# Performance work log

Hardware: AMD Instinct MI355X
Metric: run time of the kernel (lower is better)

## Reference

```python
import jax, jax.numpy as jnp
import numpy as np

NUM_HEADS = 16
NUM_KV_HEADS = 4
HEAD_DIM = 128
DIM = 2048
B, S = 2, 2048


def apply_rotary(t, cos, sin):
    # t: [B, S, H, D]; cos/sin: [S, D//2] -> broadcast [1, S, 1, D//2]
    tr = t.reshape(*t.shape[:-1], HEAD_DIM // 2, 2)
    t_r, t_i = tr[..., 0], tr[..., 1]
    c = cos[None, :, None, :]
    s = sin[None, :, None, :]
    o_r = t_r * c - t_i * s
    o_i = t_r * s + t_i * c
    return jnp.stack([o_r, o_i], axis=-1).reshape(t.shape)


def setup_inputs() -> dict:
    key = jax.random.key(0)
    ks = jax.random.split(key, 7)
    sc = 1.0 / np.sqrt(DIM)
    x = jax.random.normal(ks[0], (B, S, DIM), jnp.float32)
    pos = jnp.arange(S, dtype=jnp.float32)[:, None]
    inv_freq = 1.0 / (10000.0 ** (jnp.arange(0, HEAD_DIM, 2, dtype=jnp.float32) / HEAD_DIM))
    ang = pos * inv_freq[None, :]
    freqs_cos = jnp.cos(ang)
    freqs_sin = jnp.sin(ang)
    w_q = jax.random.normal(ks[1], (DIM, NUM_HEADS * HEAD_DIM), jnp.float32) * sc
    w_k = jax.random.normal(ks[2], (DIM, NUM_KV_HEADS * HEAD_DIM), jnp.float32) * sc
    w_v = jax.random.normal(ks[3], (DIM, NUM_KV_HEADS * HEAD_DIM), jnp.float32) * sc
    w_o = jax.random.normal(ks[4], (NUM_HEADS * HEAD_DIM, DIM), jnp.float32) * sc
    return {"x": x, "freqs_cos": freqs_cos, "freqs_sin": freqs_sin,
            "w_q": w_q, "w_k": w_k, "w_v": w_v, "w_o": w_o}


def reference(x, freqs_cos, freqs_sin, w_q, w_k, w_v, w_o):
    b, s, _ = x.shape
    kv_rep = NUM_HEADS // NUM_KV_HEADS
    q = (x @ w_q).reshape(b, s, NUM_HEADS, HEAD_DIM)
    k = (x @ w_k).reshape(b, s, NUM_KV_HEADS, HEAD_DIM)
    v = (x @ w_v).reshape(b, s, NUM_KV_HEADS, HEAD_DIM)
    q = apply_rotary(q, freqs_cos, freqs_sin)
    k = apply_rotary(k, freqs_cos, freqs_sin)
    # GQA: repeat KV heads to match query heads
    k = jnp.repeat(k, kv_rep, axis=2)
    v = jnp.repeat(v, kv_rep, axis=2)
    scores = jnp.einsum('bqhd,bkhd->bhqk', q, k) / np.sqrt(HEAD_DIM)
    causal = jnp.triu(jnp.full((s, s), -jnp.inf, jnp.float32), k=1)
    scores = scores + causal[None, None, :, :]
    attn = jax.nn.softmax(scores, axis=-1)
    out = jnp.einsum('bhqk,bkhd->bqhd', attn, v).reshape(b, s, NUM_HEADS * HEAD_DIM)
    return out @ w_o
```

## Files before the change

kernel.cpp:

```cpp
#include <hip/hip_runtime.h>
#include <stdint.h>

#define DIMSZ 2048
#define NH 16
#define NKV 4
#define HD 128
#define BATCH 2
#define SEQ 2048
#define MROWS (BATCH*SEQ)
#define NQKV (NH*HD + 2*NKV*HD)

typedef unsigned short u16;
typedef float f32x4 __attribute__((ext_vector_type(4)));
typedef short short8 __attribute__((ext_vector_type(8)));
typedef __bf16 bf16x8 __attribute__((ext_vector_type(8)));
typedef unsigned short u16x4 __attribute__((ext_vector_type(4)));

__device__ __forceinline__ u16 f2bf(float f) {
  __bf16 h = (__bf16)f;
  return __builtin_bit_cast(u16, h);
}

__device__ __forceinline__ float bf2f(u16 h) {
  union { uint32_t u; float f; } v; v.u = ((uint32_t)h) << 16; return v.f;
}

__device__ __forceinline__ void async16(void* lds, const void* g) {
  __builtin_amdgcn_global_load_lds(
      (const __attribute__((address_space(1))) void*)(g),
      (__attribute__((address_space(3))) void*)(lds), 16, 0, 0);
}

__device__ __forceinline__ bf16x8 load_frag(const u16* p) {
  short8 v = *reinterpret_cast<const short8*>(p);
  return __builtin_bit_cast(bf16x8, v);
}

__global__ void cast_x_kernel(const float* __restrict__ x, u16* __restrict__ xb) {
  int i = (blockIdx.x * blockDim.x + threadIdx.x) * 4;
  float4 v = *reinterpret_cast<const float4*>(x + i);
  u16x4 o;
  o.x = f2bf(v.x); o.y = f2bf(v.y); o.z = f2bf(v.z); o.w = f2bf(v.w);
  *reinterpret_cast<u16x4*>(xb + i) = o;
}

__global__ __launch_bounds__(1024) void wtrans_all_kernel(const float* __restrict__ wq,
                                                          const float* __restrict__ wk,
                                                          const float* __restrict__ wv,
                                                          const float* __restrict__ wo,
                                                          u16* __restrict__ wtqkv,
                                                          u16* __restrict__ wto) {
  __shared__ float t[32][33];
  int y = blockIdx.y;
  const float* src; int srcN; u16* dst; int nbase;
  if (y < 64)      { src = wq; srcN = 2048; dst = wtqkv;                          nbase = y * 32; }
  else if (y < 80) { src = wk; srcN = 512;  dst = wtqkv + (size_t)2048 * 2048;    nbase = (y - 64) * 32; }
  else if (y < 96) { src = wv; srcN = 512;  dst = wtqkv + (size_t)2560 * 2048;    nbase = (y - 80) * 32; }
  else             { src = wo; srcN = 2048; dst = wto;                            nbase = (y - 96) * 32; }
  int k0 = blockIdx.x * 32;
  int tx = threadIdx.x, ty = threadIdx.y;
  t[ty][tx] = src[(size_t)(k0 + ty) * srcN + nbase + tx];
  __syncthreads();
  dst[(size_t)(nbase + ty) * 2048 + k0 + tx] = f2bf(t[tx][ty]);
}

#define COMPUTE_PAIR(q)                                                              \
  {                                                                                  \
    bf16x8 af[2][2];                                                                 \
    _Pragma("unroll")                                                                \
    for (int m2 = 0; m2 < 2; ++m2)                                                   \
      _Pragma("unroll")                                                              \
      for (int kk = 0; kk < 2; ++kk)                                                 \
        af[m2][kk] = load_frag(&lds[buf][0][wm * 8192 +                              \
            (((q) * 2 + m2) * 16 + l16) * 64 + ((kk * 4 + lg) ^ (l16 & 7)) * 8]);    \
    __builtin_amdgcn_s_setprio(1);                                                   \
    _Pragma("unroll")                                                                \
    for (int m2 = 0; m2 < 2; ++m2)                                                   \
      _Pragma("unroll")                                                              \
      for (int ni = 0; ni < 4; ++ni)                                                 \
        _Pragma("unroll")                                                            \
        for (int kk = 0; kk < 2; ++kk)                                               \
          acc[(q) * 2 + m2][ni] = __builtin_amdgcn_mfma_f32_16x16x32_bf16(           \
              af[m2][kk], bper[ni][kk], acc[(q) * 2 + m2][ni], 0, 0, 0);             \
    __builtin_amdgcn_s_setprio(0);                                                   \
  }

template <bool BF16OUT>
__global__ __launch_bounds__(512, 2) void gemm8p_kernel(const u16* __restrict__ A,
                                                        const u16* __restrict__ BT,
                                                        void* __restrict__ Cp,
                                                        int M, int N, int K, int gx) {
  __shared__ u16 lds[2][2][16384];
  const int tid = threadIdx.x;
  const int wave = tid >> 6, lane = tid & 63;
  const int l16 = lane & 15, lg = lane >> 4;
  const int wm = wave >> 2, wn = wave & 3;
  const int rloc = lane >> 3;
  const int sOff = ((lane & 7) ^ rloc) * 8;
  const int nwg = gridDim.x;
  const int swz = (blockIdx.x & 7) * (nwg >> 3) + (blockIdx.x >> 3);
  const int bm = (swz / gx) * 256, bn = (swz % gx) * 256;

  f32x4 acc[8][4] = {};

  auto stage = [&](int dstbuf, int x, int h, const u16* xp, int xr0, int kk0) {
#pragma unroll
    for (int j = 0; j < 2; ++j) {
      int c = j * 8 + wave;
      async16(&lds[dstbuf][x][h * 8192 + c * 512],
              xp + (size_t)(xr0 + h * 128 + c * 8 + rloc) * K + kk0 + sOff);
    }
  };

  stage(0, 0, 0, A, bm, 0);
  stage(0, 0, 1, A, bm, 0);
  stage(0, 1, 0, BT, bn, 0);
  stage(0, 1, 1, BT, bn, 0);

  const int NT = K >> 6;
  for (int kt = 0; kt < NT; ++kt) {
    const int buf = kt & 1, nbuf = buf ^ 1;
    const int k0n = (kt + 1) << 6;
    const bool pf = (kt + 1 < NT);
    bf16x8 bper[4][2];

    if (pf) {
      stage(nbuf, 0, 0, A, bm, k0n);
      asm volatile("s_waitcnt vmcnt(2)" ::: "memory");
    } else {
      asm volatile("s_waitcnt vmcnt(0)" ::: "memory");
    }
    __builtin_amdgcn_s_barrier();
    __builtin_amdgcn_sched_barrier(0);
#pragma unroll
    for (int ni = 0; ni < 4; ++ni)
#pragma unroll
      for (int kk = 0; kk < 2; ++kk)
        bper[ni][kk] = load_frag(&lds[buf][1][(wn >> 1) * 8192 +
            ((wn & 1) * 64 + ni * 16 + l16) * 64 + ((kk * 4 + lg) ^ (l16 & 7)) * 8]);
    COMPUTE_PAIR(0)
    if (pf) stage(nbuf, 0, 1, A, bm, k0n);
    __builtin_amdgcn_s_barrier();
    __builtin_amdgcn_sched_barrier(0);
    COMPUTE_PAIR(1)
    if (pf) stage(nbuf, 1, 0, BT, bn, k0n);
    __builtin_amdgcn_s_barrier();
    __builtin_amdgcn_sched_barrier(0);
    COMPUTE_PAIR(2)
    if (pf) stage(nbuf, 1, 1, BT, bn, k0n);
    __builtin_amdgcn_s_barrier();
    __builtin_amdgcn_sched_barrier(0);
    COMPUTE_PAIR(3)
    __builtin_amdgcn_s_barrier();
  }

#pragma unroll
  for (int mi = 0; mi < 8; ++mi)
#pragma unroll
    for (int ni = 0; ni < 4; ++ni)
#pragma unroll
      for (int r = 0; r < 4; ++r) {
        size_t idx = (size_t)(bm + wm * 128 + mi * 16 + lg * 4 + r) * N +
                     bn + wn * 64 + ni * 16 + l16;
        if (BF16OUT) ((u16*)Cp)[idx] = f2bf(acc[mi][ni][r]);
        else         ((float*)Cp)[idx] = acc[mi][ni][r];
      }
}

template <bool BF16OUT>
__global__ __launch_bounds__(256) void gemm_bt_kernel(const u16* __restrict__ A,
                                                      const u16* __restrict__ BT,
                                                      void* __restrict__ Cp,
                                                      int M, int N, int K, int gx) {
  __shared__ u16 As[128 * 64];
  __shared__ u16 Bs[128 * 64];
  const int tid = threadIdx.x;
  const int wave = tid >> 6, lane = tid & 63;
  const int l16 = lane & 15, lg = lane >> 4;
  const int nwg = gridDim.x;
  const int swz = (blockIdx.x & 7) * (nwg >> 3) + (blockIdx.x >> 3);
  const int bm = (swz / gx) * 128, bn = (swz % gx) * 128;
  const int wrow = (wave >> 1) * 64, wcol = (wave & 1) * 64;
  int srow[4], scol[4];
#pragma unroll
  for (int i = 0; i < 4; ++i) {
    int chunk = i * 4 + wave;
    srow[i] = chunk * 8 + (lane >> 3);
    scol[i] = ((lane & 7) ^ (srow[i] & 7)) * 8;
  }
  f32x4 acc[4][4] = {};
  for (int k0 = 0; k0 < K; k0 += 64) {
    __syncthreads();
#pragma unroll
    for (int i = 0; i < 4; ++i) {
      async16(&As[(i * 4 + wave) * 512], &A[(size_t)(bm + srow[i]) * K + k0 + scol[i]]);
      async16(&Bs[(i * 4 + wave) * 512], &BT[(size_t)(bn + srow[i]) * K + k0 + scol[i]]);
    }
    __syncthreads();
#pragma unroll
    for (int kk = 0; kk < 2; ++kk) {
      bf16x8 af[4], bfr[4];
#pragma unroll
      for (int mb = 0; mb < 4; ++mb) {
        int row = wrow + mb * 16 + l16;
        af[mb] = load_frag(&As[row * 64 + ((kk * 4 + lg) ^ (row & 7)) * 8]);
      }
#pragma unroll
      for (int nb = 0; nb < 4; ++nb) {
        int row = wcol + nb * 16 + l16;
        bfr[nb] = load_frag(&Bs[row * 64 + ((kk * 4 + lg) ^ (row & 7)) * 8]);
      }
#pragma unroll
      for (int mb = 0; mb < 4; ++mb)
#pragma unroll
        for (int nb = 0; nb < 4; ++nb)
          acc[mb][nb] = __builtin_amdgcn_mfma_f32_16x16x32_bf16(af[mb], bfr[nb], acc[mb][nb], 0, 0, 0);
    }
  }
#pragma unroll
  for (int mb = 0; mb < 4; ++mb)
#pragma unroll
    for (int nb = 0; nb < 4; ++nb)
#pragma unroll
      for (int r = 0; r < 4; ++r) {
        size_t idx = (size_t)(bm + wrow + mb * 16 + lg * 4 + r) * N + bn + wcol + nb * 16 + l16;
        if (BF16OUT) ((u16*)Cp)[idx] = f2bf(acc[mb][nb][r]);
        else         ((float*)Cp)[idx] = acc[mb][nb][r];
      }
}

__global__ void rope_k_kernel(const u16* __restrict__ qkv, const float* __restrict__ fc,
                              const float* __restrict__ fs, u16* __restrict__ Kb) {
  int gi = blockIdx.x * blockDim.x + threadIdx.x;
  int i = gi & 63;
  int t = gi >> 6;
  int s = t & (SEQ - 1), b = t >> 11;
  int kh = blockIdx.y;
  float c = fc[s * 64 + i], sn = fs[s * 64 + i];
  uint32_t pr = *reinterpret_cast<const uint32_t*>(&qkv[(size_t)t * NQKV + NH * HD + kh * HD + 2 * i]);
  float tr = bf2f((u16)(pr & 0xffff)), ti = bf2f((u16)(pr >> 16));
  uint32_t w = (uint32_t)f2bf(tr * c - ti * sn) |
               ((uint32_t)f2bf(tr * sn + ti * c) << 16);
  *reinterpret_cast<uint32_t*>(&Kb[((size_t)(b * NKV + kh) * SEQ + s) * HD + 2 * i]) = w;
}

__global__ __launch_bounds__(1024) void vtrans_kernel(const u16* __restrict__ qkv,
                                                      u16* __restrict__ vt) {
  __shared__ u16 t[32][33];
  int s0 = blockIdx.x * 32, d0 = blockIdx.y * 32;
  int bk = blockIdx.z;
  int b = bk >> 2, kh = bk & 3;
  int tx = threadIdx.x, ty = threadIdx.y;
  t[ty][tx] = qkv[(size_t)(b * SEQ + s0 + ty) * NQKV + NH * HD + NKV * HD + kh * HD + d0 + tx];
  __syncthreads();
  vt[((size_t)(b * NKV + kh) * HD + d0 + ty) * SEQ + s0 + tx] = t[tx][ty];
}

__global__ __launch_bounds__(256) void attn_kernel(const u16* __restrict__ qkv,
                                                   const float* __restrict__ fc,
                                                   const float* __restrict__ fs,
                                                   const u16* __restrict__ Kc,
                                                   const u16* __restrict__ VT,
                                                   u16* __restrict__ AO) {
  __shared__ u16 Ks[2][64 * 128];
  __shared__ u16 Vs[2][128 * 64];
  __shared__ u16 Ps[4][16 * 64];
  const int pairi = blockIdx.x;
  const int h = blockIdx.y, b = blockIdx.z;
  const int kvh = h >> 2;
  const int tid = threadIdx.x, wave = tid >> 6, lane = tid & 63;
  const int l16 = lane & 15, lg = lane >> 4;

  const u16* Kbase = Kc + (size_t)(b * NKV + kvh) * SEQ * HD;
  const u16* Vbase = VT + (size_t)(b * NKV + kvh) * HD * SEQ;

  bf16x8 onesf;
#pragma unroll
  for (int j = 0; j < 8; ++j) onesf[j] = __builtin_bit_cast(__bf16, (u16)0x3F80);

  int kOff[4], vOff[4], kDst[4], vDst[4];
#pragma unroll
  for (int i = 0; i < 4; ++i) {
    int chunk = i * 4 + wave;
    int krow = chunk * 4 + (lane >> 4);
    kOff[i] = krow * HD + ((lane & 15) ^ (krow & 15)) * 8;
    kDst[i] = chunk * 512;
    int vrow = chunk * 8 + (lane >> 3);
    vOff[i] = vrow * SEQ + ((lane & 7) ^ (vrow & 7)) * 8;
    vDst[i] = chunk * 512;
  }

  for (int sel = 0; sel < 2; ++sel) {
    const int qblk = sel ? pairi : (31 - pairi);
    const int qrow0 = qblk * 64 + wave * 16;
    const int rq = qrow0 + l16;

    const float qs = 0.12751689760098266f;
    const u16* Qrow = qkv + (size_t)(b * SEQ + rq) * NQKV + h * HD;
    const float* fcb = fc + (size_t)rq * 64;
    const float* fsb = fs + (size_t)rq * 64;
    bf16x8 qf[4];
#pragma unroll
    for (int c = 0; c < 4; ++c) {
      bf16x8 raw = load_frag(Qrow + c * 32 + lg * 8);
      float4 cc = *reinterpret_cast<const float4*>(fcb + c * 16 + lg * 4);
      float4 sv = *reinterpret_cast<const float4*>(fsb + c * 16 + lg * 4);
      bf16x8 q;
#pragma unroll
      for (int j = 0; j < 4; ++j) {
        float e = (float)raw[2 * j], od = (float)raw[2 * j + 1];
        float ce = (&cc.x)[j] * qs, se = (&sv.x)[j] * qs;
        q[2 * j]     = (__bf16)(e * ce - od * se);
        q[2 * j + 1] = (__bf16)(e * se + od * ce);
      }
      qf[c] = q;
    }

    f32x4 o[8] = {};
    f32x4 lsum = {};
    float m = -3e38f;

    __syncthreads();
#pragma unroll
    for (int i = 0; i < 4; ++i) {
      async16(&Ks[0][kDst[i]], Kbase + kOff[i]);
      async16(&Vs[0][vDst[i]], Vbase + vOff[i]);
    }

    for (int kt = 0; kt <= qblk; ++kt) {
      const int cur = kt & 1;
      __syncthreads();
      if (kt < qblk) {
        const int k0n = (kt + 1) * 64;
#pragma unroll
        for (int i = 0; i < 4; ++i) {
          async16(&Ks[cur ^ 1][kDst[i]], Kbase + (size_t)k0n * HD + kOff[i]);
          async16(&Vs[cur ^ 1][vDst[i]], Vbase + k0n + vOff[i]);
        }
      }

      f32x4 s[4] = {};
      __builtin_amdgcn_s_setprio(1);
#pragma unroll
      for (int cb = 0; cb < 4; ++cb) {
#pragma unroll
        for (int c = 0; c < 4; ++c) {
          bf16x8 kf = load_frag(&Ks[cur][(cb * 16 + l16) * 128 + (((c * 4 + lg) ^ l16) & 15) * 8]);
          s[cb] = __builtin_amdgcn_mfma_f32_16x16x32_bf16(kf, qf[c], s[cb], 0, 0, 0);
        }
      }
      __builtin_amdgcn_s_setprio(0);

      if (kt == qblk) {
        const int k0 = kt * 64;
#pragma unroll
        for (int cb = 0; cb < 4; ++cb) {
#pragma unroll
          for (int r = 0; r < 4; ++r) {
            int key = k0 + cb * 16 + lg * 4 + r;
            if (key > rq) s[cb][r] = -1e30f;
          }
        }
      }

      float v0 = fmaxf(fmaxf(fmaxf(s[0][0], s[0][1]), fmaxf(s[0][2], s[0][3])),
                       fmaxf(fmaxf(s[1][0], s[1][1]), fmaxf(s[1][2], s[1][3])));
      v0 = fmaxf(v0, fmaxf(fmaxf(fmaxf(s[2][0], s[2][1]), fmaxf(s[2][2], s[2][3])),
                           fmaxf(fmaxf(s[3][0], s[3][1]), fmaxf(s[3][2], s[3][3]))));
      v0 = fmaxf(v0, __shfl_xor(v0, 16));
      v0 = fmaxf(v0, __shfl_xor(v0, 32));

      bool need = v0 > m + 8.f;
      if (__any(need)) {
        float newm = fmaxf(m, v0);
        float sc = exp2f(m - newm);
        m = newm;
        float scR[4];
#pragma unroll
        for (int r = 0; r < 4; ++r) scR[r] = __shfl(sc, lg * 4 + r);
#pragma unroll
        for (int r = 0; r < 4; ++r) {
          lsum[r] *= scR[r];
#pragma unroll
          for (int db = 0; db < 8; ++db) o[db][r] *= scR[r];
        }
      }

#pragma unroll
      for (int cb = 0; cb < 4; ++cb) {
        uint32_t lo = (uint32_t)f2bf(exp2f(s[cb][0] - m)) |
                      ((uint32_t)f2bf(exp2f(s[cb][1] - m)) << 16);
        uint32_t hi = (uint32_t)f2bf(exp2f(s[cb][2] - m)) |
                      ((uint32_t)f2bf(exp2f(s[cb][3] - m)) << 16);
        int idx = (l16 * 64 + cb * 16 + lg * 4) ^ ((l16 & 7) << 3);
        uint64_t w = (uint64_t)lo | ((uint64_t)hi << 32);
        *reinterpret_cast<uint64_t*>(&Ps[wave][idx]) = w;
      }

      bf16x8 pf[2];
#pragma unroll
      for (int c = 0; c < 2; ++c)
        pf[c] = load_frag(&Ps[wave][(l16 * 64 + c * 32 + lg * 8) ^ ((l16 & 7) << 3)]);
      __builtin_amdgcn_s_setprio(1);
#pragma unroll
      for (int c = 0; c < 2; ++c)
        lsum = __builtin_amdgcn_mfma_f32_16x16x32_bf16(pf[c], onesf, lsum, 0, 0, 0);
#pragma unroll
      for (int db = 0; db < 8; ++db) {
#pragma unroll
        for (int c = 0; c < 2; ++c) {
          bf16x8 vf = load_frag(&Vs[cur][(db * 16 + l16) * 64 + ((c * 4 + lg) ^ (l16 & 7)) * 8]);
          o[db] = __builtin_amdgcn_mfma_f32_16x16x32_bf16(pf[c], vf, o[db], 0, 0, 0);
        }
      }
      __builtin_amdgcn_s_setprio(0);
    }

#pragma unroll
    for (int r = 0; r < 4; ++r) {
      float inv = 1.f / lsum[r];
      int rqo = qrow0 + lg * 4 + r;
      size_t dst = ((size_t)(b * SEQ + rqo) * NH + h) * HD;
#pragma unroll
      for (int db = 0; db < 8; ++db)
        AO[dst + db * 16 + l16] = f2bf(o[db][r] * inv);
    }
  }
}

extern "C" void kernel_launch(void* const* d_in, const int* in_sizes, int n_in,
                              void* d_out, int out_size, void* d_ws, size_t ws_size,
                              hipStream_t stream) {
  (void)in_sizes; (void)n_in; (void)out_size; (void)ws_size;
  const float* x  = (const float*)d_in[0];
  const float* fc = (const float*)d_in[1];
  const float* fs = (const float*)d_in[2];
  const float* wq = (const float*)d_in[3];
  const float* wk = (const float*)d_in[4];
  const float* wv = (const float*)d_in[5];
  const float* wo = (const float*)d_in[6];
  float* out = (float*)d_out;

  char* ws = (char*)d_ws;
  u16*  xb    = (u16*)(ws);
  u16*  wtqkv = (u16*)(ws + 16777216);
  u16*  wto   = (u16*)(ws + 29360128);
  u16*  qkv   = (u16*)(ws + 37748736);
  u16*  Kb    = (u16*)(ws + 62914560);
  u16*  VTb   = (u16*)(ws + 67108864);
  u16*  AOb   = (u16*)(ws + 71303168);

  cast_x_kernel<<<dim3(8192), dim3(256), 0, stream>>>(x, xb);
  wtrans_all_kernel<<<dim3(64, 160), dim3(32, 32), 0, stream>>>(wq, wk, wv, wo, wtqkv, wto);

  gemm8p_kernel<true><<<dim3(192), dim3(512), 0, stream>>>(xb, wtqkv, qkv, MROWS, NQKV, DIMSZ, 12);

  rope_k_kernel<<<dim3(1024, 4), dim3(256), 0, stream>>>(qkv, fc, fs, Kb);
  vtrans_kernel<<<dim3(64, 4, 8), dim3(32, 32), 0, stream>>>(qkv, VTb);

  attn_kernel<<<dim3(16, 16, 2), dim3(256), 0, stream>>>(qkv, fc, fs, Kb, VTb, AOb);

  gemm_bt_kernel<false><<<dim3(512), dim3(256), 0, stream>>>(AOb, wto, out, MROWS, DIMSZ, DIMSZ, 16);
}
```

Baseline: 211.7 us.

## Replace output projection GEMM with double-buffered 8-wave 256x128 tile kernel

Swaps the simple 128x128 single-buffered output-projection GEMM for an 8-wave kernel using 256x128 tiles with double-buffered LDS. Async global-to-LDS loads for the next K step are interleaved between MFMA phases, with setprio raised around the MFMAs. The aim is to hide load latency behind compute and raise data reuse per tile. In exchange the block is larger and uses more LDS, and only 256 workgroups are launched, which can lower occupancy or leave some CUs idle.

```diff
diff --git a/kernel.cpp b/kernel.cpp
--- a/kernel.cpp
+++ b/kernel.cpp
@@ -167,66 +167,105 @@
       }
 }
 
-template <bool BF16OUT>
-__global__ __launch_bounds__(256) void gemm_bt_kernel(const u16* __restrict__ A,
-                                                      const u16* __restrict__ BT,
-                                                      void* __restrict__ Cp,
-                                                      int M, int N, int K, int gx) {
-  __shared__ u16 As[128 * 64];
-  __shared__ u16 Bs[128 * 64];
+#define COMPUTE_MB(q)                                                                \
+  {                                                                                  \
+    bf16x8 af[2];                                                                    \
+    _Pragma("unroll")                                                                \
+    for (int kk = 0; kk < 2; ++kk)                                                   \
+      af[kk] = load_frag(&lds2[buf][(wm * 64 + (q) * 16 + l16) * 64 +                \
+                                    ((kk * 4 + lg) ^ (l16 & 7)) * 8]);               \
+    __builtin_amdgcn_s_setprio(1);                                                   \
+    _Pragma("unroll")                                                                \
+    for (int ni = 0; ni < 4; ++ni)                                                   \
+      _Pragma("unroll")                                                              \
+      for (int kk = 0; kk < 2; ++kk)                                                 \
+        acc[(q)][ni] = __builtin_amdgcn_mfma_f32_16x16x32_bf16(                      \
+            af[kk], bper[ni][kk], acc[(q)][ni], 0, 0, 0);                            \
+    __builtin_amdgcn_s_setprio(0);                                                   \
+  }
+
+__global__ __launch_bounds__(512, 2) void gemm8p_n128_kernel(const u16* __restrict__ A,
+                                                             const u16* __restrict__ BT,
+                                                             float* __restrict__ C,
+                                                             int M, int N, int K, int gx) {
+  __shared__ u16 lds2[2][24576];
   const int tid = threadIdx.x;
   const int wave = tid >> 6, lane = tid & 63;
   const int l16 = lane & 15, lg = lane >> 4;
+  const int wm = wave >> 1, wn = wave & 1;
+  const int rloc = lane >> 3;
+  const int sOff = ((lane & 7) ^ rloc) * 8;
   const int nwg = gridDim.x;
   const int swz = (blockIdx.x & 7) * (nwg >> 3) + (blockIdx.x >> 3);
-  const int bm = (swz / gx) * 128, bn = (swz % gx) * 128;
-  const int wrow = (wave >> 1) * 64, wcol = (wave & 1) * 64;
-  int srow[4], scol[4];
-#pragma unroll
-  for (int i = 0; i < 4; ++i) {
-    int chunk = i * 4 + wave;
-    srow[i] = chunk * 8 + (lane >> 3);
-    scol[i] = ((lane & 7) ^ (srow[i] & 7)) * 8;
+  const int bm = (swz / gx) * 256, bn = (swz % gx) * 128;
+
+  f32x4 acc[4][4] = {};
+
+  auto stageA = [&](int dstbuf, int h, int kk0) {
+#pragma unroll
+    for (int j = 0; j < 2; ++j) {
+      int c = j * 8 + wave;
+      async16(&lds2[dstbuf][h * 8192 + c * 512],
+              A + (size_t)(bm + h * 128 + c * 8 + rloc) * K + kk0 + sOff);
+    }
+  };
+  auto stageB = [&](int dstbuf, int kk0) {
+#pragma unroll
+    for (int j = 0; j < 2; ++j) {
+      int c = j * 8 + wave;
+      async16(&lds2[dstbuf][16384 + c * 512],
+              BT + (size_t)(bn + c * 8 + rloc) * K + kk0 + sOff);
+    }
+  };
+
+  stageA(0, 0, 0);
+  stageA(0, 1, 0);
+  stageB(0, 0);
+
+  const int NT = K >> 6;
+  for (int kt = 0; kt < NT; ++kt) {
+    const int buf = kt & 1, nbuf = buf ^ 1;
+    const int k0n = (kt + 1) << 6;
+    const bool pf = (kt + 1 < NT);
+    bf16x8 bper[4][2];
+
+    if (pf) {
+      stageA(nbuf, 0, k0n);
+      asm volatile("s_waitcnt vmcnt(2)" ::: "memory");
+    } else {
+      asm volatile("s_waitcnt vmcnt(0)" ::: "memory");
+    }
+    __builtin_amdgcn_s_barrier();
+    __builtin_amdgcn_sched_barrier(0);
+#pragma unroll
+    for (int ni = 0; ni < 4; ++ni)
+#pragma unroll
+      for (int kk = 0; kk < 2; ++kk)
+        bper[ni][kk] = load_frag(&lds2[buf][16384 +
+            (wn * 64 + ni * 16 + l16) * 64 + ((kk * 4 + lg) ^ (l16 & 7)) * 8]);
+    COMPUTE_MB(0)
+    if (pf) stageA(nbuf, 1, k0n);
+    __builtin_amdgcn_s_barrier();
+    __builtin_amdgcn_sched_barrier(0);
+    COMPUTE_MB(1)
+    if (pf) stageB(nbuf, k0n);
+    __builtin_amdgcn_s_barrier();
+    __builtin_amdgcn_sched_barrier(0);
+    COMPUTE_MB(2)
+    __builtin_amdgcn_s_barrier();
+    __builtin_amdgcn_sched_barrier(0);
+    COMPUTE_MB(3)
+    __builtin_amdgcn_s_barrier();
   }
-  f32x4 acc[4][4] = {};
-  for (int k0 = 0; k0 < K; k0 += 64) {
-    __syncthreads();
-#pragma unroll
-    for (int i = 0; i < 4; ++i) {
-      async16(&As[(i * 4 + wave) * 512], &A[(size_t)(bm + srow[i]) * K + k0 + scol[i]]);
-      async16(&Bs[(i * 4 + wave) * 512], &BT[(size_t)(bn + srow[i]) * K + k0 + scol[i]]);
-    }
-    __syncthreads();
-#pragma unroll
-    for (int kk = 0; kk < 2; ++kk) {
-      bf16x8 af[4], bfr[4];
-#pragma unroll
-      for (int mb = 0; mb < 4; ++mb) {
-        int row = wrow + mb * 16 + l16;
-        af[mb] = load_frag(&As[row * 64 + ((kk * 4 + lg) ^ (row & 7)) * 8]);
-      }
-#pragma unroll
-      for (int nb = 0; nb < 4; ++nb) {
-        int row = wcol + nb * 16 + l16;
-        bfr[nb] = load_frag(&Bs[row * 64 + ((kk * 4 + lg) ^ (row & 7)) * 8]);
-      }
-#pragma unroll
-      for (int mb = 0; mb < 4; ++mb)
-#pragma unroll
-        for (int nb = 0; nb < 4; ++nb)
-          acc[mb][nb] = __builtin_amdgcn_mfma_f32_16x16x32_bf16(af[mb], bfr[nb], acc[mb][nb], 0, 0, 0);
-    }
-  }
+
 #pragma unroll
   for (int mb = 0; mb < 4; ++mb)
 #pragma unroll
-    for (int nb = 0; nb < 4; ++nb)
-#pragma unroll
-      for (int r = 0; r < 4; ++r) {
-        size_t idx = (size_t)(bm + wrow + mb * 16 + lg * 4 + r) * N + bn + wcol + nb * 16 + l16;
-        if (BF16OUT) ((u16*)Cp)[idx] = f2bf(acc[mb][nb][r]);
-        else         ((float*)Cp)[idx] = acc[mb][nb][r];
-      }
+    for (int ni = 0; ni < 4; ++ni)
+#pragma unroll
+      for (int r = 0; r < 4; ++r)
+        C[(size_t)(bm + wm * 64 + mb * 16 + lg * 4 + r) * N +
+          bn + wn * 64 + ni * 16 + l16] = acc[mb][ni][r];
 }
 
 __global__ void rope_k_kernel(const u16* __restrict__ qkv, const float* __restrict__ fc,
@@ -460,5 +499,5 @@
 
   attn_kernel<<<dim3(16, 16, 2), dim3(256), 0, stream>>>(qkv, fc, fs, Kb, VTb, AOb);
 
-  gemm_bt_kernel<false><<<dim3(512), dim3(256), 0, stream>>>(AOb, wto, out, MROWS, DIMSZ, DIMSZ, 16);
-}
+  gemm8p_n128_kernel<<<dim3(256), dim3(512), 0, stream>>>(AOb, wto, out, MROWS, DIMSZ, DIMSZ, 16);
+}
```

Result: faster. 206.8 us (-2.3%).
